# Performance work log

Measured on AMD Instinct MI355X. Metric: run time of the kernel, lower is better.

The kernel has to match this reference:

```python
import jax, jax.numpy as jnp
import numpy as np

NUM_QUESTION = 10000


def setup_inputs() -> dict:
    key = jax.random.key(0)
    ks = jax.random.split(key, 12)
    B, L, DK, SLOTS = 64, 200, 128, 64
    return {
        "question_seq": jax.random.randint(ks[0], (B, L), 0, NUM_QUESTION),
        "correct_seq": jax.random.randint(ks[1], (B, L), 0, 2),
        "q_emb": jax.random.normal(ks[2], (NUM_QUESTION, DK), jnp.float32) * 0.05,
        "v_emb": jax.random.normal(ks[3], (2 * NUM_QUESTION, DK), jnp.float32) * 0.05,
        "Mk": jax.random.normal(ks[4], (SLOTS, DK), jnp.float32) * 0.1,
        "Mv0": jax.random.normal(ks[5], (SLOTS, DK), jnp.float32) * 0.1,
        "eW": jax.random.normal(ks[6], (DK, DK), jnp.float32) * 0.05,
        "eb": jnp.zeros((DK,), jnp.float32),
        "aW": jax.random.normal(ks[7], (DK, DK), jnp.float32) * 0.05,
        "ab": jnp.zeros((DK,), jnp.float32),
        "fW": jax.random.normal(ks[8], (DK, 2 * DK), jnp.float32) * 0.05,
        "fb": jnp.zeros((DK,), jnp.float32),
        "pW": jax.random.normal(ks[9], (1, DK), jnp.float32) * 0.05,
        "pb": jnp.zeros((1,), jnp.float32),
    }


def reference(question_seq, correct_seq, q_emb, v_emb, Mk, Mv0,
              eW, eb, aW, ab, fW, fb, pW, pb):
    B = question_seq.shape[0]
    x = question_seq + NUM_QUESTION * correct_seq          # [B, L]
    k = q_emb[question_seq]                                # [B, L, DK]
    v = v_emb[x]                                           # [B, L, DK]
    w = jax.nn.softmax(jnp.einsum("bld,sd->bls", k, Mk), axis=-1)  # [B, L, S]
    e = jax.nn.sigmoid(v @ eW.T + eb)                      # [B, L, DK]
    a = jnp.tanh(v @ aW.T + ab)                            # [B, L, DK]

    Mv_init = jnp.broadcast_to(Mv0[None], (B,) + Mv0.shape)  # [B, S, DK]

    def step(Mvt, inp):
        wt, et, at = inp  # [B,S], [B,DK], [B,DK]
        # read uses memory BEFORE the write (Mv[:, :-1] in the original)
        read = jnp.einsum("bs,bsd->bd", wt, Mvt)
        we = wt[:, :, None]
        Mvt = Mvt * (1.0 - we * et[:, None, :]) + we * at[:, None, :]
        return Mvt, read

    xs = (w.transpose(1, 0, 2), e.transpose(1, 0, 2), a.transpose(1, 0, 2))
    _, reads = jax.lax.scan(step, Mv_init, xs)             # reads: [L, B, DK]
    reads = reads.transpose(1, 0, 2)                       # [B, L, DK]

    f = jnp.tanh(jnp.concatenate([reads, k], axis=-1) @ fW.T + fb)
    predict_score = jax.nn.sigmoid(f @ pW.T + pb)[..., 0]  # [B, L]
    return predict_score
```

## Files before the change

kernel.cpp:

```cpp
#include <hip/hip_runtime.h>
#include <hip/hip_bf16.h>

#define NQ 10000
#define BATCH 64
#define SEQL 200
#define DKD 128
#define SLOTS 64
#define NTOK (BATCH*SEQL)

typedef __attribute__((ext_vector_type(8))) short bh8;
typedef __attribute__((ext_vector_type(4))) float f32x4;
typedef unsigned short u16;
typedef unsigned int u32;

__device__ __forceinline__ float sigmoidf_(float x){ return 1.0f/(1.0f + __expf(-x)); }
__device__ __forceinline__ float tanhf_(float x){
  float ax = fminf(fabsf(x), 30.0f);
  float t = __expf(-2.0f*ax);
  float r = (1.0f-t)/(1.0f+t);
  return copysignf(r, x);
}
__device__ __forceinline__ u16 f2b(float x){
  u32 u = __builtin_bit_cast(u32, x);
  u32 r = (u + 0x7FFFu + ((u >> 16) & 1u)) >> 16;
  return (u16)r;
}
__device__ __forceinline__ bh8 cvt8(const float* s){
  float4 v0 = *(const float4*)s, v1 = *(const float4*)(s + 4);
  bh8 h;
  h[0]=(short)f2b(v0.x); h[1]=(short)f2b(v0.y); h[2]=(short)f2b(v0.z); h[3]=(short)f2b(v0.w);
  h[4]=(short)f2b(v1.x); h[5]=(short)f2b(v1.y); h[6]=(short)f2b(v1.z); h[7]=(short)f2b(v1.w);
  return h;
}
__device__ __forceinline__ int swz(int row, int col16, int rowBytes){
  return row*rowBytes + ((col16 ^ (row & 7)) << 4);
}

__global__ __launch_bounds__(512) void wea_kernel(
    const int* __restrict__ qseq, const int* __restrict__ cseq,
    const float* __restrict__ q_emb, const float* __restrict__ v_emb,
    const float* __restrict__ Mk, const float* __restrict__ eW,
    const float* __restrict__ aW,
    const float* __restrict__ eb, const float* __restrict__ ab,
    float* __restrict__ w_out, float* __restrict__ e_out, float* __restrict__ a_out)
{
  __shared__ __align__(16) char smem[73728];
  char* As = smem;
  char* Bs = smem + 8192;
  float* Ls = (float*)(smem + 24576);

  const int tid = threadIdx.x;
  const int l = tid & 63, wv = tid >> 6;
  const bool isW = (blockIdx.x < 400);
  const int tok0 = (isW ? blockIdx.x : blockIdx.x - 400) * 32;

  {
    int row = tid >> 4, c16 = tid & 15;
    const float* src;
    if (isW){ int q = qseq[tok0+row]; src = q_emb + (size_t)q*DKD + c16*8; }
    else    { int x = qseq[tok0+row] + NQ*cseq[tok0+row]; src = v_emb + (size_t)x*DKD + c16*8; }
    *(bh8*)(As + swz(row, c16, 256)) = cvt8(src);
  }
  if (isW){
    #pragma unroll
    for (int m = 0; m < 2; ++m){
      int idx = tid + 512*m; int row = idx >> 4, c16 = idx & 15;
      *(bh8*)(Bs + swz(row, c16, 256)) = cvt8(Mk + (size_t)row*DKD + c16*8);
    }
  } else {
    #pragma unroll
    for (int m = 0; m < 8; ++m){
      int idx = tid + 512*m; int row = idx >> 4, c16 = idx & 15;
      const float* src = (row < 128) ? (eW + (size_t)row*DKD) : (aW + (size_t)(row-128)*DKD);
      *(bh8*)(Bs + swz(row, c16, 256)) = cvt8(src + c16*8);
    }
  }
  __syncthreads();

  if (isW){
    const int m = wv & 1, n = wv >> 1;
    f32x4 acc = {0.f,0.f,0.f,0.f};
    #pragma unroll
    for (int kc = 0; kc < 4; ++kc){
      bh8 af = *(const bh8*)(As + swz(m*16 + (l&15), kc*4 + (l>>4), 256));
      bh8 bf = *(const bh8*)(Bs + swz(n*16 + (l&15), kc*4 + (l>>4), 256));
      acc = __builtin_amdgcn_mfma_f32_16x16x32_bf16(af, bf, acc, 0, 0, 0);
    }
    #pragma unroll
    for (int r = 0; r < 4; ++r){
      int tok = m*16 + (l>>4)*4 + r, out = n*16 + (l&15);
      Ls[tok*68 + out] = acc[r];
    }
    __syncthreads();
    #pragma unroll
    for (int i = 0; i < 4; ++i){
      int tok = wv*4 + i;
      float x = Ls[tok*68 + l];
      float mx = x;
      #pragma unroll
      for (int off = 32; off >= 1; off >>= 1) mx = fmaxf(mx, __shfl_xor(mx, off));
      float p = __expf(x - mx);
      float s = p;
      #pragma unroll
      for (int off = 32; off >= 1; off >>= 1) s += __shfl_xor(s, off);
      w_out[(size_t)(tok0+tok)*SLOTS + l] = p / s;
    }
  } else {
    const int m = wv & 1, nq = (wv >> 1) * 4;
    f32x4 acc[4] = {{0.f,0.f,0.f,0.f},{0.f,0.f,0.f,0.f},{0.f,0.f,0.f,0.f},{0.f,0.f,0.f,0.f}};
    #pragma unroll
    for (int kc = 0; kc < 4; ++kc){
      bh8 af = *(const bh8*)(As + swz(m*16 + (l&15), kc*4 + (l>>4), 256));
      #pragma unroll
      for (int j = 0; j < 4; ++j){
        bh8 bf = *(const bh8*)(Bs + swz((nq+j)*16 + (l&15), kc*4 + (l>>4), 256));
        acc[j] = __builtin_amdgcn_mfma_f32_16x16x32_bf16(af, bf, acc[j], 0, 0, 0);
      }
    }
    #pragma unroll
    for (int j = 0; j < 4; ++j){
      int out = (nq+j)*16 + (l&15);
      bool is_e = (out < 128);
      int d = out & 127;
      float bias = is_e ? eb[d] : ab[d];
      #pragma unroll
      for (int r = 0; r < 4; ++r){
        int tok = tok0 + m*16 + (l>>4)*4 + r;
        float xv = acc[j][r] + bias;
        if (is_e) e_out[(size_t)tok*DKD + d] = sigmoidf_(xv);
        else      a_out[(size_t)tok*DKD + d] = tanhf_(xv);
      }
    }
  }
}

__device__ __forceinline__ float dpp_row_sum16(float x){
  float t;
  t = __builtin_bit_cast(float, __builtin_amdgcn_update_dpp(0, __builtin_bit_cast(int,x), 0x111, 0xf, 0xf, true)); x += t;
  t = __builtin_bit_cast(float, __builtin_amdgcn_update_dpp(0, __builtin_bit_cast(int,x), 0x112, 0xf, 0xf, true)); x += t;
  t = __builtin_bit_cast(float, __builtin_amdgcn_update_dpp(0, __builtin_bit_cast(int,x), 0x114, 0xf, 0xf, true)); x += t;
  t = __builtin_bit_cast(float, __builtin_amdgcn_update_dpp(0, __builtin_bit_cast(int,x), 0x118, 0xf, 0xf, true)); x += t;
  return x;
}

#define TC 32
#define NCHUNK 7

__global__ __launch_bounds__(256) void scan_kernel(
    const float* __restrict__ Mv0,
    const float* __restrict__ w_in, const float* __restrict__ e_in,
    const float* __restrict__ a_in, u16* __restrict__ r16)
{
  __shared__ float wS[2][TC][64];
  __shared__ float eS[2][16][36];
  __shared__ float aS[2][16][36];
  const int tid = threadIdx.x;
  const int b  = blockIdx.x >> 3;
  const int d0 = (blockIdx.x & 7) << 4;
  const int c  = tid >> 4;
  const int g  = tid & 15;
  const int d  = d0 + c;

  float mv0 = Mv0[(4*g+0)*DKD + d];
  float mv1 = Mv0[(4*g+1)*DKD + d];
  float mv2 = Mv0[(4*g+2)*DKD + d];
  float mv3 = Mv0[(4*g+3)*DKD + d];

  const int st_t = tid & 31;
  const int st_j = tid >> 5;
  const float4* wsrc = (const float4*)(w_in + (size_t)b*SEQL*SLOTS);
  const float*  ebase = e_in + ((size_t)b*SEQL + st_t)*DKD + d0;
  const float*  abase = a_in + ((size_t)b*SEQL + st_t)*DKD + d0;
  u16* rp = r16 + (size_t)b*SEQL*DKD + d;
  const bool wlane = (g == 15);

  {
    float4 wA = wsrc[tid], wB = wsrc[tid + 256];
    float e0 = ebase[st_j],     e1 = ebase[st_j + 8];
    float a0 = abase[st_j],     a1 = abase[st_j + 8];
    ((float4*)wS[0])[tid] = wA; ((float4*)wS[0])[tid + 256] = wB;
    eS[0][st_j][st_t] = e0; eS[0][st_j+8][st_t] = e1;
    aS[0][st_j][st_t] = a0; aS[0][st_j+8][st_t] = a1;
    __syncthreads();
  }

  int cur = 0;
  for (int ck = 0; ck < NCHUNK; ++ck){
    const int T0 = ck * TC;
    float4 wA, wB; float e0, e1, a0, a1;
    if (ck < NCHUNK-1){
      const int T0n = T0 + TC;
      wA = wsrc[T0n*16 + tid]; wB = wsrc[T0n*16 + tid + 256];
      e0 = ebase[(size_t)T0n*DKD + st_j]; e1 = ebase[(size_t)T0n*DKD + st_j + 8];
      a0 = abase[(size_t)T0n*DKD + st_j]; a1 = abase[(size_t)T0n*DKD + st_j + 8];
    }
    #pragma unroll
    for (int u = 0; u < TC/4; ++u){
      float eq[4], aq[4];
      *(float4*)eq = *(const float4*)&eS[cur][c][u*4];
      *(float4*)aq = *(const float4*)&aS[cur][c][u*4];
      #pragma unroll
      for (int v = 0; v < 4; ++v){
        const int tt = u*4 + v;
        float4 wq = *(const float4*)&wS[cur][tt][g*4];
        float r = wq.x*mv0; r = fmaf(wq.y, mv1, r); r = fmaf(wq.z, mv2, r); r = fmaf(wq.w, mv3, r);
        r = dpp_row_sum16(r);
        if ((T0 + tt) < SEQL && wlane) rp[(size_t)(T0+tt)*DKD] = f2b(r);
        const float ev = eq[v], av = aq[v];
        mv0 = fmaf(wq.x, fmaf(-mv0, ev, av), mv0);
        mv1 = fmaf(wq.y, fmaf(-mv1, ev, av), mv1);
        mv2 = fmaf(wq.z, fmaf(-mv2, ev, av), mv2);
        mv3 = fmaf(wq.w, fmaf(-mv3, ev, av), mv3);
      }
    }
    if (ck < NCHUNK-1){
      ((float4*)wS[cur^1])[tid] = wA; ((float4*)wS[cur^1])[tid + 256] = wB;
      eS[cur^1][st_j][st_t] = e0; eS[cur^1][st_j+8][st_t] = e1;
      aS[cur^1][st_j][st_t] = a0; aS[cur^1][st_j+8][st_t] = a1;
      __syncthreads();
      cur ^= 1;
    }
  }
}

__global__ __launch_bounds__(512) void p3_kernel(
    const int* __restrict__ qseq, const float* __restrict__ q_emb,
    const u16* __restrict__ r16, const float* __restrict__ fW,
    const float* __restrict__ fb, const float* __restrict__ pW,
    const float* __restrict__ pb, float* __restrict__ out)
{
  __shared__ __align__(16) char smem[81920];
  char* As = smem;
  char* Bs = smem + 16384;

  const int tid = threadIdx.x;
  const int l = tid & 63, wv = tid >> 6;
  const int tok0 = blockIdx.x * 32;

  #pragma unroll
  for (int m = 0; m < 2; ++m){
    int idx = tid + 512*m; int row = idx >> 5, c16 = idx & 31;
    bh8 v;
    if (c16 < 16){
      v = *(const bh8*)(r16 + (size_t)(tok0+row)*DKD + c16*8);
    } else {
      int q = qseq[tok0+row];
      v = cvt8(q_emb + (size_t)q*DKD + (c16-16)*8);
    }
    *(bh8*)(As + swz(row, c16, 512)) = v;
  }
  #pragma unroll
  for (int m = 0; m < 8; ++m){
    int idx = tid + 512*m; int row = idx >> 5, c16 = idx & 31;
    *(bh8*)(Bs + swz(row, c16, 512)) = cvt8(fW + (size_t)row*256 + c16*8);
  }
  __syncthreads();

  const int m = wv & 1, np = (wv >> 1) * 2;
  f32x4 acc[2] = {{0.f,0.f,0.f,0.f},{0.f,0.f,0.f,0.f}};
  #pragma unroll
  for (int kc = 0; kc < 8; ++kc){
    bh8 af = *(const bh8*)(As + swz(m*16 + (l&15), kc*4 + (l>>4), 512));
    #pragma unroll
    for (int j = 0; j < 2; ++j){
      bh8 bf = *(const bh8*)(Bs + swz((np+j)*16 + (l&15), kc*4 + (l>>4), 512));
      acc[j] = __builtin_amdgcn_mfma_f32_16x16x32_bf16(af, bf, acc[j], 0, 0, 0);
    }
  }
  float pp[4] = {0.f,0.f,0.f,0.f};
  #pragma unroll
  for (int j = 0; j < 2; ++j){
    int o = (np+j)*16 + (l&15);
    float bias = fb[o], pw = pW[o];
    #pragma unroll
    for (int r = 0; r < 4; ++r){
      float f = tanhf_(acc[j][r] + bias);
      pp[r] = fmaf(f, pw, pp[r]);
    }
  }
  #pragma unroll
  for (int r = 0; r < 4; ++r){
    pp[r] += __shfl_xor(pp[r], 1);
    pp[r] += __shfl_xor(pp[r], 2);
    pp[r] += __shfl_xor(pp[r], 4);
    pp[r] += __shfl_xor(pp[r], 8);
  }
  __syncthreads();
  float* pbuf = (float*)smem;
  if ((l & 15) == 0){
    #pragma unroll
    for (int r = 0; r < 4; ++r){
      int tok = m*16 + (l>>4)*4 + r;
      pbuf[wv*32 + tok] = pp[r];
    }
  }
  __syncthreads();
  if (tid < 32){
    int mm = tid >> 4;
    float s = pbuf[(mm+0)*32 + tid] + pbuf[(mm+2)*32 + tid]
            + pbuf[(mm+4)*32 + tid] + pbuf[(mm+6)*32 + tid];
    out[tok0 + tid] = sigmoidf_(s + pb[0]);
  }
}

extern "C" void kernel_launch(void* const* d_in, const int* in_sizes, int n_in,
                              void* d_out, int out_size, void* d_ws, size_t ws_size,
                              hipStream_t stream) {
  const int*   qseq  = (const int*)d_in[0];
  const int*   cseq  = (const int*)d_in[1];
  const float* q_emb = (const float*)d_in[2];
  const float* v_emb = (const float*)d_in[3];
  const float* Mk    = (const float*)d_in[4];
  const float* Mv0   = (const float*)d_in[5];
  const float* eW    = (const float*)d_in[6];
  const float* eb    = (const float*)d_in[7];
  const float* aW    = (const float*)d_in[8];
  const float* ab    = (const float*)d_in[9];
  const float* fW    = (const float*)d_in[10];
  const float* fb    = (const float*)d_in[11];
  const float* pW    = (const float*)d_in[12];
  const float* pb    = (const float*)d_in[13];

  char* ws = (char*)d_ws;
  float* w_buf = (float*)ws;
  float* e_buf = (float*)(ws + 3276800);
  float* a_buf = (float*)(ws + 9830400);
  u16*   r16   = (u16*)  (ws + 16384000);
  float* outp  = (float*)d_out;

  hipLaunchKernelGGL(wea_kernel, dim3(800), dim3(512), 0, stream,
                     qseq, cseq, q_emb, v_emb, Mk, eW, aW, eb, ab,
                     w_buf, e_buf, a_buf);
  hipLaunchKernelGGL(scan_kernel, dim3(512), dim3(256), 0, stream,
                     Mv0, w_buf, e_buf, a_buf, r16);
  hipLaunchKernelGGL(p3_kernel, dim3(NTOK/32), dim3(512), 0, stream,
                     qseq, q_emb, r16, fW, fb, pW, pb, outp);
}
```

Before: 57.31 us.

## Transpose e/a to per-batch dim-major layout and restructure scan pipelining

```diff
diff --git a/kernel.cpp b/kernel.cpp
--- a/kernel.cpp
+++ b/kernel.cpp
@@ -42,7 +42,7 @@
     const float* __restrict__ Mk, const float* __restrict__ eW,
     const float* __restrict__ aW,
     const float* __restrict__ eb, const float* __restrict__ ab,
-    float* __restrict__ w_out, float* __restrict__ e_out, float* __restrict__ a_out)
+    float* __restrict__ w_out, float* __restrict__ eT, float* __restrict__ aT)
 {
   __shared__ __align__(16) char smem[73728];
   char* As = smem;
@@ -121,15 +121,18 @@
     for (int j = 0; j < 4; ++j){
       int out = (nq+j)*16 + (l&15);
       bool is_e = (out < 128);
-      int d = out & 127;
-      float bias = is_e ? eb[d] : ab[d];
+      int dd = out & 127;
+      float bias = is_e ? eb[dd] : ab[dd];
+      float4 sv;
       #pragma unroll
       for (int r = 0; r < 4; ++r){
-        int tok = tok0 + m*16 + (l>>4)*4 + r;
         float xv = acc[j][r] + bias;
-        if (is_e) e_out[(size_t)tok*DKD + d] = sigmoidf_(xv);
-        else      a_out[(size_t)tok*DKD + d] = tanhf_(xv);
+        ((float*)&sv)[r] = is_e ? sigmoidf_(xv) : tanhf_(xv);
       }
+      int tg = tok0 + m*16 + (l>>4)*4;
+      int bb = tg / SEQL, tl = tg - bb*SEQL;
+      float* dst = (is_e ? eT : aT) + ((size_t)bb*DKD + dd)*SEQL + tl;
+      *(float4*)dst = sv;
     }
   }
 }
@@ -143,84 +146,100 @@
   return x;
 }
 
-#define TC 32
-#define NCHUNK 7
+#define TCH 8
+#define NCH 25
 
 __global__ __launch_bounds__(256) void scan_kernel(
     const float* __restrict__ Mv0,
-    const float* __restrict__ w_in, const float* __restrict__ e_in,
-    const float* __restrict__ a_in, u16* __restrict__ r16)
+    const float* __restrict__ w_in, const float* __restrict__ eT,
+    const float* __restrict__ aT, u16* __restrict__ r16)
 {
-  __shared__ float wS[2][TC][64];
-  __shared__ float eS[2][16][36];
-  __shared__ float aS[2][16][36];
+  __shared__ float eaS[2][2][16][8];
+  __shared__ float rbuf[2][TCH][16];
   const int tid = threadIdx.x;
   const int b  = blockIdx.x >> 3;
   const int d0 = (blockIdx.x & 7) << 4;
   const int c  = tid >> 4;
   const int g  = tid & 15;
   const int d  = d0 + c;
+  const bool wlane = (g == 15);
 
   float mv0 = Mv0[(4*g+0)*DKD + d];
   float mv1 = Mv0[(4*g+1)*DKD + d];
   float mv2 = Mv0[(4*g+2)*DKD + d];
   float mv3 = Mv0[(4*g+3)*DKD + d];
 
-  const int st_t = tid & 31;
-  const int st_j = tid >> 5;
   const float4* wsrc = (const float4*)(w_in + (size_t)b*SEQL*SLOTS);
-  const float*  ebase = e_in + ((size_t)b*SEQL + st_t)*DKD + d0;
-  const float*  abase = a_in + ((size_t)b*SEQL + st_t)*DKD + d0;
-  u16* rp = r16 + (size_t)b*SEQL*DKD + d;
-  const bool wlane = (g == 15);
+  const int sdd = (tid & 127) >> 3, sth = tid & 7;
+  const float* easrc = ((tid < 128) ? eT : aT) + ((size_t)b*DKD + d0 + sdd)*SEQL + sth;
+  const int sarr = (tid < 128) ? 1 : 0;
+  u16* rp = r16 + (size_t)b*SEQL*DKD + d0;
+
+  float4 wA[TCH], wB[TCH];
 
   {
-    float4 wA = wsrc[tid], wB = wsrc[tid + 256];
-    float e0 = ebase[st_j],     e1 = ebase[st_j + 8];
-    float a0 = abase[st_j],     a1 = abase[st_j + 8];
-    ((float4*)wS[0])[tid] = wA; ((float4*)wS[0])[tid + 256] = wB;
-    eS[0][st_j][st_t] = e0; eS[0][st_j+8][st_t] = e1;
-    aS[0][st_j][st_t] = a0; aS[0][st_j+8][st_t] = a1;
+    #pragma unroll
+    for (int i = 0; i < TCH; ++i) wA[i] = wsrc[i*16 + g];
+    float ea0 = easrc[0];
+    eaS[0][(tid < 128) ? 0 : 1][sdd][sth] = ea0;
     __syncthreads();
   }
 
-  int cur = 0;
-  for (int ck = 0; ck < NCHUNK; ++ck){
-    const int T0 = ck * TC;
-    float4 wA, wB; float e0, e1, a0, a1;
-    if (ck < NCHUNK-1){
-      const int T0n = T0 + TC;
-      wA = wsrc[T0n*16 + tid]; wB = wsrc[T0n*16 + tid + 256];
-      e0 = ebase[(size_t)T0n*DKD + st_j]; e1 = ebase[(size_t)T0n*DKD + st_j + 8];
-      a0 = abase[(size_t)T0n*DKD + st_j]; a1 = abase[(size_t)T0n*DKD + st_j + 8];
-    }
-    #pragma unroll
-    for (int u = 0; u < TC/4; ++u){
-      float eq[4], aq[4];
-      *(float4*)eq = *(const float4*)&eS[cur][c][u*4];
-      *(float4*)aq = *(const float4*)&aS[cur][c][u*4];
-      #pragma unroll
-      for (int v = 0; v < 4; ++v){
-        const int tt = u*4 + v;
-        float4 wq = *(const float4*)&wS[cur][tt][g*4];
-        float r = wq.x*mv0; r = fmaf(wq.y, mv1, r); r = fmaf(wq.z, mv2, r); r = fmaf(wq.w, mv3, r);
-        r = dpp_row_sum16(r);
-        if ((T0 + tt) < SEQL && wlane) rp[(size_t)(T0+tt)*DKD] = f2b(r);
-        const float ev = eq[v], av = aq[v];
-        mv0 = fmaf(wq.x, fmaf(-mv0, ev, av), mv0);
-        mv1 = fmaf(wq.y, fmaf(-mv1, ev, av), mv1);
-        mv2 = fmaf(wq.z, fmaf(-mv2, ev, av), mv2);
-        mv3 = fmaf(wq.w, fmaf(-mv3, ev, av), mv3);
-      }
-    }
-    if (ck < NCHUNK-1){
-      ((float4*)wS[cur^1])[tid] = wA; ((float4*)wS[cur^1])[tid + 256] = wB;
-      eS[cur^1][st_j][st_t] = e0; eS[cur^1][st_j+8][st_t] = e1;
-      aS[cur^1][st_j][st_t] = a0; aS[cur^1][st_j+8][st_t] = a1;
-      __syncthreads();
-      cur ^= 1;
-    }
-  }
+  #define COMPUTE(P, WC)                                                  \
+    _Pragma("unroll")                                                     \
+    for (int u = 0; u < 2; ++u){                                          \
+      float eq[4], aq[4];                                                 \
+      *(float4*)eq = *(const float4*)&eaS[P][0][c][u*4];                  \
+      *(float4*)aq = *(const float4*)&eaS[P][1][c][u*4];                  \
+      _Pragma("unroll")                                                   \
+      for (int v = 0; v < 4; ++v){                                        \
+        const int tt = u*4 + v;                                           \
+        float4 wq = WC[tt];                                               \
+        float r = wq.x*mv0; r = fmaf(wq.y, mv1, r);                       \
+        r = fmaf(wq.z, mv2, r); r = fmaf(wq.w, mv3, r);                   \
+        r = dpp_row_sum16(r);                                             \
+        if (wlane) rbuf[P][tt][c] = r;                                    \
+        const float ev = eq[v], av = aq[v];                               \
+        mv0 = fmaf(wq.x, fmaf(-mv0, ev, av), mv0);                        \
+        mv1 = fmaf(wq.y, fmaf(-mv1, ev, av), mv1);                        \
+        mv2 = fmaf(wq.z, fmaf(-mv2, ev, av), mv2);                        \
+        mv3 = fmaf(wq.w, fmaf(-mv3, ev, av), mv3);                        \
+      }                                                                   \
+    }
+
+  #define STORER(CK, P)                                                  \
+    if (tid < 64){                                                       \
+      int t = tid >> 3, dp = tid & 7;                                    \
+      float2 rv = *(const float2*)&rbuf[P][t][dp*2];                     \
+      u32 pk = (u32)f2b(rv.x) | ((u32)f2b(rv.y) << 16);                  \
+      *(u32*)(rp + (size_t)((CK)*TCH + t)*DKD + dp*2) = pk;              \
+    }
+
+  #define PHASE(CK, P, WC, WN)                                           \
+    {                                                                    \
+      if ((CK) > 0) STORER((CK)-1, (P)^1);                               \
+      const int T0n = ((CK)+1)*TCH;                                      \
+      _Pragma("unroll")                                                  \
+      for (int i = 0; i < TCH; ++i) WN[i] = wsrc[(T0n+i)*16 + g];        \
+      float ean = easrc[T0n];                                            \
+      COMPUTE(P, WC)                                                     \
+      eaS[(P)^1][(tid < 128) ? 0 : 1][sdd][sth] = ean;                   \
+      __syncthreads();                                                   \
+    }
+
+  for (int ck = 0; ck < 24; ck += 2){
+    PHASE(ck,   0, wA, wB)
+    PHASE(ck+1, 1, wB, wA)
+  }
+  STORER(23, 1);
+  COMPUTE(0, wA)
+  __syncthreads();
+  STORER(24, 0);
+
+  #undef COMPUTE
+  #undef STORER
+  #undef PHASE
+  (void)sarr;
 }
 
 __global__ __launch_bounds__(512) void p3_kernel(
@@ -323,16 +342,16 @@
 
   char* ws = (char*)d_ws;
   float* w_buf = (float*)ws;
-  float* e_buf = (float*)(ws + 3276800);
-  float* a_buf = (float*)(ws + 9830400);
+  float* eT    = (float*)(ws + 3276800);
+  float* aT    = (float*)(ws + 9830400);
   u16*   r16   = (u16*)  (ws + 16384000);
   float* outp  = (float*)d_out;
 
   hipLaunchKernelGGL(wea_kernel, dim3(800), dim3(512), 0, stream,
                      qseq, cseq, q_emb, v_emb, Mk, eW, aW, eb, ab,
-                     w_buf, e_buf, a_buf);
+                     w_buf, eT, aT);
   hipLaunchKernelGGL(scan_kernel, dim3(512), dim3(256), 0, stream,
-                     Mv0, w_buf, e_buf, a_buf, r16);
+                     Mv0, w_buf, eT, aT, r16);
   hipLaunchKernelGGL(p3_kernel, dim3(NTOK/32), dim3(512), 0, stream,
                      qseq, q_emb, r16, fW, fb, pW, pb, outp);
 }
```

After: 50.62 us. -11.7%, faster.
